# Kernel optimization log

Measured on AMD Instinct MI355X. Metric: run time of the kernel, lower is better.

The kernel has to match this reference:

```python
import jax, jax.numpy as jnp
import numpy as np

N_NODES = 50000
N_EDGES = 1600000
IN_DIM = 512
OUT_DIM = 256
SCALING_FACTOR = 1.8


def setup_inputs() -> dict:
    key = jax.random.key(0)
    k1, k2, k3, k4 = jax.random.split(key, 4)
    x = jax.random.normal(k1, (N_NODES, IN_DIM), dtype=jnp.float32)
    W = jax.random.normal(k2, (OUT_DIM, IN_DIM), dtype=jnp.float32) * (1.0 / np.sqrt(IN_DIM))
    b = jax.random.normal(k3, (OUT_DIM,), dtype=jnp.float32) * 0.01
    edge_index = jax.random.randint(k4, (2, N_EDGES), 0, N_NODES, dtype=jnp.int64)
    return {"x": x, "W": W, "b": b, "edge_index": edge_index}


def reference(x, W, b, edge_index):
    N = x.shape[0]
    # Linear
    z = x @ W.T + b  # [N, out_dim]
    # L2 normalize per row (torch F.normalize eps=1e-12) then scale
    nrm = jnp.sqrt(jnp.sum(z * z, axis=1, keepdims=True))
    z = z / jnp.maximum(nrm, 1e-12) * SCALING_FACTOR
    # APPNP(K=1, alpha=0) == one GCN-normalized hop with self-loops
    loop = jnp.arange(N, dtype=edge_index.dtype)
    src = jnp.concatenate([edge_index[0], loop])
    dst = jnp.concatenate([edge_index[1], loop])
    deg = jax.ops.segment_sum(jnp.ones(src.shape[0], z.dtype), dst, num_segments=N)
    dis = jax.lax.rsqrt(deg)  # deg >= 1 due to self-loops
    norm = dis[src] * dis[dst]  # [E+N]
    out = jax.ops.segment_sum(norm[:, None] * z[src], dst, num_segments=N)  # [N, out_dim]
    return out
```

## Files before the change

### kernel.cpp

```cpp
#include <hip/hip_runtime.h>
#include <cstdint>
#include <cstddef>

#define IN_DIM 512
#define OUT_DIM 256
#define SCALE 1.8f

typedef __bf16 bf16x8 __attribute__((ext_vector_type(8)));
typedef float f32x4 __attribute__((ext_vector_type(4)));

__device__ __forceinline__ float bf_lo(unsigned u) { return __uint_as_float(u << 16); }
__device__ __forceinline__ float bf_hi(unsigned u) { return __uint_as_float(u & 0xffff0000u); }

__global__ void detect_kernel(const int* __restrict__ ei, int* __restrict__ flag) {
    int t = threadIdx.x;
    int nz = (ei[2 * t + 1] != 0) ? 1 : 0;
    unsigned long long b = __ballot(nz);
    if (t == 0) *flag = (b == 0ULL) ? 1 : 0;
}

__global__ void zero_i32(int* __restrict__ p, int n) {
    int i = blockIdx.x * blockDim.x + threadIdx.x;
    if (i < n) p[i] = 0;
}

__global__ void convert_w(const float* __restrict__ W, __bf16* __restrict__ Bh,
                          __bf16* __restrict__ Bl) {
    int t = blockIdx.x * blockDim.x + threadIdx.x;
    if (t >= OUT_DIM * (IN_DIM / 8)) return;
    int n = t >> 6, kc = t & 63;
    float4 p0 = *(const float4*)&W[(size_t)n * IN_DIM + kc * 8];
    float4 p1 = *(const float4*)&W[(size_t)n * IN_DIM + kc * 8 + 4];
    float v[8] = {p0.x, p0.y, p0.z, p0.w, p1.x, p1.y, p1.z, p1.w};
    int nt = n >> 4, k0 = kc >> 2;
    int lane = ((kc & 3) << 4) | (n & 15);
    size_t slot = ((size_t)(k0 * 16 + nt) * 64 + lane) * 8;
    bf16x8 hv, lv;
#pragma unroll
    for (int j = 0; j < 8; ++j) {
        __bf16 h = (__bf16)v[j];
        hv[j] = h;
        lv[j] = (__bf16)(v[j] - (float)h);
    }
    *(bf16x8*)&Bh[slot] = hv;
    *(bf16x8*)&Bl[slot] = lv;
}

__global__ void count_kernel(const int* __restrict__ ei32, const long long* __restrict__ ei64,
                             const int* __restrict__ flag, int* __restrict__ cnt, int E) {
    bool w64 = (*flag != 0);
    int stride = gridDim.x * blockDim.x;
    for (int e = blockIdx.x * blockDim.x + threadIdx.x; e < E; e += stride) {
        int d = w64 ? (int)ei64[(size_t)E + e] : ei32[(size_t)E + e];
        atomicAdd(&cnt[d], 1);
    }
}

__global__ void dis_kernel(const int* __restrict__ cnt, float* __restrict__ dis, int N) {
    int i = blockIdx.x * blockDim.x + threadIdx.x;
    if (i < N) dis[i] = 1.0f / sqrtf((float)(cnt[i] + 1));
}

__global__ void scan1_kernel(const int* __restrict__ cnt, int* __restrict__ tmp,
                             int* __restrict__ bsum, int N) {
    __shared__ int s[256];
    int t = threadIdx.x;
    int i = blockIdx.x * 256 + t;
    s[t] = (i < N) ? cnt[i] : 0;
    __syncthreads();
    for (int off = 1; off < 256; off <<= 1) {
        int add = (t >= off) ? s[t - off] : 0;
        __syncthreads();
        s[t] += add;
        __syncthreads();
    }
    if (i < N) tmp[i] = s[t];
    if (t == 255) bsum[blockIdx.x] = s[255];
}

__global__ void scan2_kernel(const int* __restrict__ bsum, int* __restrict__ bscan, int NB) {
    __shared__ int s[256];
    int t = threadIdx.x;
    s[t] = (t < NB) ? bsum[t] : 0;
    __syncthreads();
    for (int off = 1; off < 256; off <<= 1) {
        int add = (t >= off) ? s[t - off] : 0;
        __syncthreads();
        s[t] += add;
        __syncthreads();
    }
    bscan[t] = s[t];
}

__global__ void finalize_kernel(const int* __restrict__ tmp, const int* __restrict__ bscan,
                                const int* __restrict__ cnt, int* __restrict__ rowptr,
                                int* __restrict__ cursor, int N) {
    int i = blockIdx.x * blockDim.x + threadIdx.x;
    if (i < N) {
        int base = (i >= 256) ? bscan[(i >> 8) - 1] : 0;
        int endv = tmp[i] + base;
        rowptr[i + 1] = endv;
        cursor[i] = endv - cnt[i];
        if (i == 0) rowptr[0] = 0;
    }
}

__global__ void fill_kernel(const int* __restrict__ ei32, const long long* __restrict__ ei64,
                            const int* __restrict__ flag, int* __restrict__ cursor,
                            int* __restrict__ col, int E) {
    bool w64 = (*flag != 0);
    int stride = gridDim.x * blockDim.x;
    for (int e = blockIdx.x * blockDim.x + threadIdx.x; e < E; e += stride) {
        int s, d;
        if (w64) { s = (int)ei64[e]; d = (int)ei64[(size_t)E + e]; }
        else     { s = ei32[e];      d = ei32[(size_t)E + e]; }
        int pos = atomicAdd(&cursor[d], 1);
        col[pos] = s;
    }
}

__global__ __launch_bounds__(256, 2) void mfma_gemm(
    const float* __restrict__ x, const bf16x8* __restrict__ Bh8,
    const bf16x8* __restrict__ Bl8, const float* __restrict__ bias,
    const float* __restrict__ dis, __bf16* __restrict__ y, int Nn, int MT)
{
    const int lane = threadIdx.x & 63;
    const int rt = blockIdx.x * 4 + (threadIdx.x >> 6);
    if (rt >= MT) return;

    f32x4 acc[16];
#pragma unroll
    for (int nt = 0; nt < 16; ++nt) acc[nt] = (f32x4){0.f, 0.f, 0.f, 0.f};

    const int row = rt * 16 + (lane & 15);
    const float* xp = x + (size_t)(row < Nn ? row : 0) * IN_DIM + ((lane >> 4) * 8);

#pragma unroll 2
    for (int k0 = 0; k0 < 16; ++k0) {
        float4 p0 = *(const float4*)(xp + k0 * 32);
        float4 p1 = *(const float4*)(xp + k0 * 32 + 4);
        float av[8] = {p0.x, p0.y, p0.z, p0.w, p1.x, p1.y, p1.z, p1.w};
        bf16x8 ah, al;
#pragma unroll
        for (int j = 0; j < 8; ++j) {
            __bf16 h = (__bf16)av[j];
            ah[j] = h;
            al[j] = (__bf16)(av[j] - (float)h);
        }
        const bf16x8* bh = Bh8 + (size_t)(k0 * 16) * 64 + lane;
        const bf16x8* bl = Bl8 + (size_t)(k0 * 16) * 64 + lane;
#pragma unroll
        for (int nt = 0; nt < 16; ++nt) {
            bf16x8 vh = bh[nt * 64];
            bf16x8 vl = bl[nt * 64];
            acc[nt] = __builtin_amdgcn_mfma_f32_16x16x32_bf16(ah, vh, acc[nt], 0, 0, 0);
            acc[nt] = __builtin_amdgcn_mfma_f32_16x16x32_bf16(al, vh, acc[nt], 0, 0, 0);
            acc[nt] = __builtin_amdgcn_mfma_f32_16x16x32_bf16(ah, vl, acc[nt], 0, 0, 0);
        }
    }

    const int col0 = lane & 15;
    float ss[4] = {0.f, 0.f, 0.f, 0.f};
#pragma unroll
    for (int nt = 0; nt < 16; ++nt) {
        float bb = bias[nt * 16 + col0];
#pragma unroll
        for (int j = 0; j < 4; ++j) {
            acc[nt][j] += bb;
            ss[j] = fmaf(acc[nt][j], acc[nt][j], ss[j]);
        }
    }
#pragma unroll
    for (int m = 1; m <= 8; m <<= 1) {
#pragma unroll
        for (int j = 0; j < 4; ++j) ss[j] += __shfl_xor(ss[j], m);
    }
    const int rbase = rt * 16 + (lane >> 4) * 4;
#pragma unroll
    for (int j = 0; j < 4; ++j) {
        int r = rbase + j;
        if (r < Nn) {
            float sc = SCALE * dis[r] / fmaxf(sqrtf(ss[j]), 1e-12f);
#pragma unroll
            for (int nt = 0; nt < 16; ++nt)
                y[(size_t)r * OUT_DIM + nt * 16 + col0] = (__bf16)(acc[nt][j] * sc);
        }
    }
}

__global__ __launch_bounds__(256) void gather_kernel(
    const uint2* __restrict__ y2, const int* __restrict__ rowptr,
    const int* __restrict__ col, const float* __restrict__ dis,
    float4* __restrict__ out4, int Nn)
{
    const int lane = threadIdx.x & 63;
    const int wid = (blockIdx.x * blockDim.x + threadIdx.x) >> 6;
    const int nw = (gridDim.x * blockDim.x) >> 6;
    for (int n = wid; n < Nn; n += nw) {
        const int beg = rowptr[n], end = rowptr[n + 1];
        uint2 v = y2[(size_t)n * 64 + lane];
        float a0 = bf_lo(v.x), a1 = bf_hi(v.x), a2 = bf_lo(v.y), a3 = bf_hi(v.y);
        int j = beg;
        for (; j + 1 < end; j += 2) {
            int s0 = col[j], s1 = col[j + 1];
            uint2 u0 = y2[(size_t)s0 * 64 + lane];
            uint2 u1 = y2[(size_t)s1 * 64 + lane];
            a0 += bf_lo(u0.x) + bf_lo(u1.x);
            a1 += bf_hi(u0.x) + bf_hi(u1.x);
            a2 += bf_lo(u0.y) + bf_lo(u1.y);
            a3 += bf_hi(u0.y) + bf_hi(u1.y);
        }
        if (j < end) {
            uint2 u = y2[(size_t)col[j] * 64 + lane];
            a0 += bf_lo(u.x); a1 += bf_hi(u.x);
            a2 += bf_lo(u.y); a3 += bf_hi(u.y);
        }
        float dn = dis[n];
        out4[(size_t)n * 64 + lane] = make_float4(a0 * dn, a1 * dn, a2 * dn, a3 * dn);
    }
}

extern "C" void kernel_launch(void* const* d_in, const int* in_sizes, int n_in,
                              void* d_out, int out_size, void* d_ws, size_t ws_size,
                              hipStream_t stream) {
    const float* x = (const float*)d_in[0];
    const float* W = (const float*)d_in[1];
    const float* b = (const float*)d_in[2];
    const int* ei32 = (const int*)d_in[3];
    const long long* ei64 = (const long long*)d_in[3];
    const int N = in_sizes[0] / IN_DIM;
    const int E = in_sizes[3] / 2;
    const int MT = (N + 15) / 16;
    float* out = (float*)d_out;

    char* ws = (char*)d_ws;
    size_t off = 0;
    auto alloc = [&](size_t bytes) -> void* {
        void* p = ws + off;
        off = (off + bytes + 255) & ~(size_t)255;
        return p;
    };
    __bf16* y    = (__bf16*)alloc((size_t)MT * 16 * OUT_DIM * sizeof(__bf16));
    __bf16* Bh   = (__bf16*)alloc((size_t)IN_DIM * OUT_DIM * sizeof(__bf16));
    __bf16* Bl   = (__bf16*)alloc((size_t)IN_DIM * OUT_DIM * sizeof(__bf16));
    float* dis   = (float*)alloc((size_t)N * sizeof(float));
    int*   cnt   = (int*)alloc((size_t)N * sizeof(int));
    int*   tmp   = (int*)alloc((size_t)N * sizeof(int));
    int*   rowptr= (int*)alloc((size_t)(N + 1) * sizeof(int));
    int*   cursor= (int*)alloc((size_t)N * sizeof(int));
    int*   bsum  = (int*)alloc(512 * sizeof(int));
    int*   bscan = (int*)alloc(512 * sizeof(int));
    int*   flag  = (int*)alloc(sizeof(int));
    int*   col   = (int*)alloc((size_t)E * sizeof(int));
    (void)ws_size; (void)n_in; (void)out_size;

    const int NB = (N + 255) >> 8;

    hipLaunchKernelGGL(detect_kernel, dim3(1), dim3(64), 0, stream, ei32, flag);
    hipLaunchKernelGGL(zero_i32, dim3((N + 255) / 256), dim3(256), 0, stream, cnt, N);
    hipLaunchKernelGGL(convert_w, dim3((OUT_DIM * (IN_DIM / 8) + 255) / 256), dim3(256), 0, stream, W, Bh, Bl);
    hipLaunchKernelGGL(count_kernel, dim3(2048), dim3(256), 0, stream, ei32, ei64, flag, cnt, E);
    hipLaunchKernelGGL(dis_kernel, dim3((N + 255) / 256), dim3(256), 0, stream, cnt, dis, N);
    hipLaunchKernelGGL(scan1_kernel, dim3(NB), dim3(256), 0, stream, cnt, tmp, bsum, N);
    hipLaunchKernelGGL(scan2_kernel, dim3(1), dim3(256), 0, stream, bsum, bscan, NB);
    hipLaunchKernelGGL(finalize_kernel, dim3((N + 255) / 256), dim3(256), 0, stream, tmp, bscan, cnt, rowptr, cursor, N);
    hipLaunchKernelGGL(fill_kernel, dim3(2048), dim3(256), 0, stream, ei32, ei64, flag, cursor, col, E);
    hipLaunchKernelGGL(mfma_gemm, dim3((MT + 3) / 4), dim3(256), 0, stream,
                       x, (const bf16x8*)Bh, (const bf16x8*)Bl, b, dis, y, N, MT);
    hipLaunchKernelGGL(gather_kernel, dim3(2048), dim3(256), 0, stream,
                       (const uint2*)y, rowptr, col, dis, (float4*)out, N);
}
```

Baseline: 640.4 us.

## Stage GEMM weight tiles in LDS with double-buffered async loads; fold dis into finalize

The GEMM now loads the hi/lo bf16 weight slices for each K step into shared memory using global_load_lds, double-buffered so the next slice streams in while the current one feeds MFMAs. All four waves in a block share the staged weights, where before each wave read them from global/L2 itself. A block-wide barrier is added per K step, and the early return for out-of-range waves is removed so the barrier stays uniform. Separately, the degree-normalisation computation is merged into finalize_kernel, dropping one kernel launch.

```diff
diff --git a/kernel.cpp b/kernel.cpp
--- a/kernel.cpp
+++ b/kernel.cpp
@@ -8,6 +8,13 @@
 
 typedef __bf16 bf16x8 __attribute__((ext_vector_type(8)));
 typedef float f32x4 __attribute__((ext_vector_type(4)));
+
+typedef const __attribute__((address_space(1))) unsigned int* gas1_t;
+typedef __attribute__((address_space(3))) unsigned int* as3_t;
+
+__device__ __forceinline__ void gload_lds16(const void* g, void* l) {
+    __builtin_amdgcn_global_load_lds((gas1_t)g, (as3_t)l, 16, 0, 0);
+}
 
 __device__ __forceinline__ float bf_lo(unsigned u) { return __uint_as_float(u << 16); }
 __device__ __forceinline__ float bf_hi(unsigned u) { return __uint_as_float(u & 0xffff0000u); }
@@ -56,11 +63,6 @@
     }
 }
 
-__global__ void dis_kernel(const int* __restrict__ cnt, float* __restrict__ dis, int N) {
-    int i = blockIdx.x * blockDim.x + threadIdx.x;
-    if (i < N) dis[i] = 1.0f / sqrtf((float)(cnt[i] + 1));
-}
-
 __global__ void scan1_kernel(const int* __restrict__ cnt, int* __restrict__ tmp,
                              int* __restrict__ bsum, int N) {
     __shared__ int s[256];
@@ -94,13 +96,15 @@
 
 __global__ void finalize_kernel(const int* __restrict__ tmp, const int* __restrict__ bscan,
                                 const int* __restrict__ cnt, int* __restrict__ rowptr,
-                                int* __restrict__ cursor, int N) {
+                                int* __restrict__ cursor, float* __restrict__ dis, int N) {
     int i = blockIdx.x * blockDim.x + threadIdx.x;
     if (i < N) {
+        int c = cnt[i];
         int base = (i >= 256) ? bscan[(i >> 8) - 1] : 0;
         int endv = tmp[i] + base;
         rowptr[i + 1] = endv;
-        cursor[i] = endv - cnt[i];
+        cursor[i] = endv - c;
+        dis[i] = 1.0f / sqrtf((float)(c + 1));
         if (i == 0) rowptr[0] = 0;
     }
 }
@@ -120,13 +124,28 @@
 }
 
 __global__ __launch_bounds__(256, 2) void mfma_gemm(
-    const float* __restrict__ x, const bf16x8* __restrict__ Bh8,
-    const bf16x8* __restrict__ Bl8, const float* __restrict__ bias,
+    const float* __restrict__ x, const __bf16* __restrict__ Bh,
+    const __bf16* __restrict__ Bl, const float* __restrict__ bias,
     const float* __restrict__ dis, __bf16* __restrict__ y, int Nn, int MT)
 {
-    const int lane = threadIdx.x & 63;
-    const int rt = blockIdx.x * 4 + (threadIdx.x >> 6);
-    if (rt >= MT) return;
+    __shared__ __align__(16) __bf16 lds[2][2][8192];
+    const int tid  = threadIdx.x;
+    const int lane = tid & 63;
+    const int w    = tid >> 6;
+    const int rt   = blockIdx.x * 4 + w;
+
+    auto stage = [&](int p, int k0) {
+        const __bf16* sH = Bh + (size_t)k0 * 8192;
+        const __bf16* sL = Bl + (size_t)k0 * 8192;
+#pragma unroll
+        for (int i = 0; i < 4; ++i) {
+            int chunk = w * 4 + i;
+            size_t goff = ((size_t)chunk * 64 + lane) * 8;
+            size_t loff = (size_t)chunk * 64 * 8;
+            gload_lds16(sH + goff, &lds[p][0][loff]);
+            gload_lds16(sL + goff, &lds[p][1][loff]);
+        }
+    };
 
     f32x4 acc[16];
 #pragma unroll
@@ -135,8 +154,13 @@
     const int row = rt * 16 + (lane & 15);
     const float* xp = x + (size_t)(row < Nn ? row : 0) * IN_DIM + ((lane >> 4) * 8);
 
-#pragma unroll 2
+    stage(0, 0);
+    __syncthreads();
+
     for (int k0 = 0; k0 < 16; ++k0) {
+        const int p = k0 & 1;
+        if (k0 < 15) stage(p ^ 1, k0 + 1);
+
         float4 p0 = *(const float4*)(xp + k0 * 32);
         float4 p1 = *(const float4*)(xp + k0 * 32 + 4);
         float av[8] = {p0.x, p0.y, p0.z, p0.w, p1.x, p1.y, p1.z, p1.w};
@@ -147,16 +171,17 @@
             ah[j] = h;
             al[j] = (__bf16)(av[j] - (float)h);
         }
-        const bf16x8* bh = Bh8 + (size_t)(k0 * 16) * 64 + lane;
-        const bf16x8* bl = Bl8 + (size_t)(k0 * 16) * 64 + lane;
+        const __bf16* bH = &lds[p][0][0];
+        const __bf16* bL = &lds[p][1][0];
 #pragma unroll
         for (int nt = 0; nt < 16; ++nt) {
-            bf16x8 vh = bh[nt * 64];
-            bf16x8 vl = bl[nt * 64];
+            bf16x8 vh = *(const bf16x8*)(bH + (((size_t)nt * 64 + lane) << 3));
+            bf16x8 vl = *(const bf16x8*)(bL + (((size_t)nt * 64 + lane) << 3));
             acc[nt] = __builtin_amdgcn_mfma_f32_16x16x32_bf16(ah, vh, acc[nt], 0, 0, 0);
             acc[nt] = __builtin_amdgcn_mfma_f32_16x16x32_bf16(al, vh, acc[nt], 0, 0, 0);
             acc[nt] = __builtin_amdgcn_mfma_f32_16x16x32_bf16(ah, vl, acc[nt], 0, 0, 0);
         }
+        __syncthreads();
     }
 
     const int col0 = lane & 15;
@@ -260,13 +285,12 @@
     hipLaunchKernelGGL(zero_i32, dim3((N + 255) / 256), dim3(256), 0, stream, cnt, N);
     hipLaunchKernelGGL(convert_w, dim3((OUT_DIM * (IN_DIM / 8) + 255) / 256), dim3(256), 0, stream, W, Bh, Bl);
     hipLaunchKernelGGL(count_kernel, dim3(2048), dim3(256), 0, stream, ei32, ei64, flag, cnt, E);
-    hipLaunchKernelGGL(dis_kernel, dim3((N + 255) / 256), dim3(256), 0, stream, cnt, dis, N);
     hipLaunchKernelGGL(scan1_kernel, dim3(NB), dim3(256), 0, stream, cnt, tmp, bsum, N);
     hipLaunchKernelGGL(scan2_kernel, dim3(1), dim3(256), 0, stream, bsum, bscan, NB);
-    hipLaunchKernelGGL(finalize_kernel, dim3((N + 255) / 256), dim3(256), 0, stream, tmp, bscan, cnt, rowptr, cursor, N);
+    hipLaunchKernelGGL(finalize_kernel, dim3((N + 255) / 256), dim3(256), 0, stream, tmp, bscan, cnt, rowptr, cursor, dis, N);
     hipLaunchKernelGGL(fill_kernel, dim3(2048), dim3(256), 0, stream, ei32, ei64, flag, cursor, col, E);
     hipLaunchKernelGGL(mfma_gemm, dim3((MT + 3) / 4), dim3(256), 0, stream,
-                       x, (const bf16x8*)Bh, (const bf16x8*)Bl, b, dis, y, N, MT);
+                       x, Bh, Bl, b, dis, y, N, MT);
     hipLaunchKernelGGL(gather_kernel, dim3(2048), dim3(256), 0, stream,
                        (const uint2*)y, rowptr, col, dis, (float4*)out, N);
 }
```

New measurement: 552.0 us. -13.8%, faster.
